# Optimization experiments

Measured on AMD Instinct MI355X. Metric: run time of the kernel, lower is better.

Reference implementation:

```python
import jax, jax.numpy as jnp
import numpy as np

BT = 64  # chunk size (BLOCK_SIZE_C)
EPS = 1e-06


def setup_inputs() -> dict:
    key = jax.random.key(0)
    k1, k2, k3, k4 = jax.random.split(key, 4)
    B, H, S, D = 4, 8, 4096, 128
    q = jax.random.normal(k1, (B, H, S, D), dtype=jnp.float32)
    k = jax.random.normal(k2, (B, H, S, D), dtype=jnp.float32)
    v = jax.random.normal(k3, (B, H, S, D), dtype=jnp.float32)
    beta = jax.random.uniform(k4, (B, H, S), dtype=jnp.float32)
    return {"q": q, "k": k, "v": v, "beta": beta}


def _chunk_gated_delta_fwd(q, k, v, beta):
    # Recurrence: S_t = beta_t * S_{t-1} + k_t (x) v_t ;  o_t = q_t @ S_t
    B, H, S, D = q.shape
    NC = S // BT
    f32 = jnp.float32
    qf = q.astype(f32).reshape(B, H, NC, BT, D)
    kf = k.astype(f32).reshape(B, H, NC, BT, D)
    vf = v.astype(f32).reshape(B, H, NC, BT, D)
    log_beta = jnp.log(beta.astype(f32).reshape(B, H, NC, BT) + EPS)
    cum = jnp.cumsum(log_beta, axis=-1)                     # [B,H,NC,BT]
    tot = cum[..., -1]                                      # [B,H,NC]
    decay_from_start = jnp.exp(cum)                         # [B,H,NC,BT]
    decay_to_end = jnp.exp(tot[..., None] - cum)            # [B,H,NC,BT]
    causal = jnp.tril(jnp.ones((BT, BT), dtype=bool))
    decay_matrix = jnp.exp(cum[..., :, None] - cum[..., None, :])  # [B,H,NC,BT,BT]
    decay_masked = jnp.where(causal, decay_matrix, 0.0)
    # intra-chunk contribution (fully parallel across chunks)
    qk = jnp.einsum('bhcid,bhcjd->bhcij', qf, kf)
    out_intra = jnp.einsum('bhcij,bhcjd->bhcid', qk * decay_masked, vf)
    # per-chunk state-update term: (k * decay_to_end)^T @ v
    upd = jnp.einsum('bhcid,bhcie->bhcde', kf * decay_to_end[..., None], vf)
    # sequential inter-chunk recurrence over chunks
    def step(state, xs):
        qc, dfs_c, tot_c, upd_c = xs
        out_inter = jnp.einsum('bhid,bhde->bhie', qc * dfs_c[..., None], state)
        new_state = state * jnp.exp(tot_c)[..., None, None] + upd_c
        return new_state, out_inter
    xs = (jnp.moveaxis(qf, 2, 0), jnp.moveaxis(decay_from_start, 2, 0),
          jnp.moveaxis(tot, 2, 0), jnp.moveaxis(upd, 2, 0))
    state0 = jnp.zeros((B, H, D, D), dtype=f32)
    _, out_inter = jax.lax.scan(step, state0, xs)           # [NC,B,H,BT,D]
    out = out_intra + jnp.moveaxis(out_inter, 0, 2)
    return out.reshape(B, H, S, D).astype(q.dtype)


def reference(q, k, v, beta):
    return _chunk_gated_delta_fwd(q, k, v, beta)
```

## Files before the change

kernel.cpp:

```cpp
#include <hip/hip_runtime.h>
#include <hip/hip_bf16.h>
#include <math.h>

#define Gp  32
#define Sp  4096
#define Dp  128
#define BTp 64
#define NCp 64

typedef __attribute__((ext_vector_type(8))) short bf16x8;
typedef __attribute__((ext_vector_type(4))) float f32x4;

#define MFMA(a,b,c) __builtin_amdgcn_mfma_f32_16x16x32_bf16((a),(b),(c),0,0,0)

#define TSWZ(d, slot) ((((slot) ^ (((d) & 15) >> 1)) << 3))

__device__ inline unsigned pack2(float lo, float hi) {
    __hip_bfloat162 h = __float22bfloat162_rn(make_float2(lo, hi));
    union { __hip_bfloat162 v; unsigned u; } t; t.v = h; return t.u;
}
__device__ inline float bflo(unsigned u) { union { unsigned u; float f; } t; t.u = u << 16; return t.f; }
__device__ inline float bfhi(unsigned u) { union { unsigned u; float f; } t; t.u = u & 0xffff0000u; return t.f; }

__global__ __launch_bounds__(256, 3) void gdn_intra(
    const float* __restrict__ q, const float* __restrict__ k,
    const float* __restrict__ v, const float* __restrict__ beta,
    float* __restrict__ out, unsigned short* __restrict__ upd,
    float* __restrict__ tot_buf, float* __restrict__ dfs_buf)
{
    __shared__ unsigned short s_k [64 * 128];
    __shared__ unsigned short s_vt[128 * 64];
    __shared__ unsigned short s_kt[128 * 64];

    const int blk = blockIdx.x, g = blk >> 6, c = blk & 63;
    const int tid = threadIdx.x, lane = tid & 63, w = tid >> 6;
    const int m16 = lane & 15, quad = lane >> 4;
    const size_t base  = ((size_t)g * Sp + (size_t)c * BTp) * Dp;
    const size_t bbase = (size_t)g * Sp + (size_t)c * BTp;

    float x = logf(beta[bbase + lane] + 1e-6f);
    #pragma unroll
    for (int off = 1; off < 64; off <<= 1) {
        float n = __shfl_up(x, off, 64);
        if (lane >= off) x += n;
    }
    const float tot = __shfl(x, 63, 64);
    const float dte_own = expf(tot - x);
    if (tid < 64) dfs_buf[bbase + lane] = expf(x);
    if (tid == 63) tot_buf[g * NCp + c] = tot;

    bf16x8 qf[4];
    {
        const float* qrow = q + base + (size_t)(16 * w + m16) * Dp + quad * 8;
        #pragma unroll
        for (int ks = 0; ks < 4; ++ks) {
            const float4 a = *(const float4*)(qrow + ks * 32);
            const float4 b = *(const float4*)(qrow + ks * 32 + 4);
            union { bf16x8 v; unsigned ui[4]; } t;
            t.ui[0] = pack2(a.x, a.y); t.ui[1] = pack2(a.z, a.w);
            t.ui[2] = pack2(b.x, b.y); t.ui[3] = pack2(b.z, b.w);
            qf[ks] = t.v;
        }
    }

    #pragma unroll
    for (int it = 0; it < 8; ++it) {
        const int idx = (it * 256 + tid) * 4;
        const int i = idx >> 7, d = idx & 127;
        const float4 kv = *(const float4*)(k + base + (size_t)i * Dp + d);
        const int ad = i * 128 + (((d >> 3) ^ (i & 15)) << 3) + (d & 7);
        uint2 pw; pw.x = pack2(kv.x, kv.y); pw.y = pack2(kv.z, kv.w);
        *(uint2*)&s_k[ad] = pw;
    }

    #pragma unroll
    for (int it = 0; it < 2; ++it) {
        const int dd = 2 * (tid & 63);
        const int i  = 32 * it + 8 * w;
        float2 lv[8], lk[8];
        #pragma unroll
        for (int r = 0; r < 8; ++r) {
            lv[r] = *(const float2*)(v + base + (size_t)(i + r) * Dp + dd);
            lk[r] = *(const float2*)(k + base + (size_t)(i + r) * Dp + dd);
        }
        float dt[8];
        #pragma unroll
        for (int r = 0; r < 8; ++r) dt[r] = __shfl(dte_own, i + r, 64);
        const int sl = TSWZ(dd, i >> 3);
        uint4 t0, t1;
        t0.x = pack2(lv[0].x, lv[1].x); t0.y = pack2(lv[2].x, lv[3].x);
        t0.z = pack2(lv[4].x, lv[5].x); t0.w = pack2(lv[6].x, lv[7].x);
        t1.x = pack2(lv[0].y, lv[1].y); t1.y = pack2(lv[2].y, lv[3].y);
        t1.z = pack2(lv[4].y, lv[5].y); t1.w = pack2(lv[6].y, lv[7].y);
        *(uint4*)&s_vt[dd * 64 + sl]       = t0;
        *(uint4*)&s_vt[(dd + 1) * 64 + sl] = t1;
        t0.x = pack2(lk[0].x * dt[0], lk[1].x * dt[1]); t0.y = pack2(lk[2].x * dt[2], lk[3].x * dt[3]);
        t0.z = pack2(lk[4].x * dt[4], lk[5].x * dt[5]); t0.w = pack2(lk[6].x * dt[6], lk[7].x * dt[7]);
        t1.x = pack2(lk[0].y * dt[0], lk[1].y * dt[1]); t1.y = pack2(lk[2].y * dt[2], lk[3].y * dt[3]);
        t1.z = pack2(lk[4].y * dt[4], lk[5].y * dt[5]); t1.w = pack2(lk[6].y * dt[6], lk[7].y * dt[7]);
        *(uint4*)&s_kt[dd * 64 + sl]       = t0;
        *(uint4*)&s_kt[(dd + 1) * 64 + sl] = t1;
    }

    __syncthreads();

    f32x4 accP[4] = {};
    #pragma unroll
    for (int nt = 0; nt < 4; ++nt) {
        if (nt <= w) {
            #pragma unroll
            for (int ks = 0; ks < 4; ++ks) {
                const bf16x8 kf = *(const bf16x8*)&s_k[(16 * nt + m16) * 128 + (((quad + 4 * ks) ^ m16) << 3)];
                accP[nt] = MFMA(kf, qf[ks], accP[nt]);
            }
        }
    }

    const float ci = __shfl(x, 16 * w + m16, 64);
    unsigned p_pk[4][2];
    #pragma unroll
    for (int nt = 0; nt < 4; ++nt) { p_pk[nt][0] = 0u; p_pk[nt][1] = 0u; }
    #pragma unroll
    for (int nt = 0; nt < 4; ++nt) {
        if (nt <= w) {
            float pm[4];
            #pragma unroll
            for (int r = 0; r < 4; ++r) {
                const int j = 16 * nt + 4 * quad + r;
                const float cj = __shfl(x, j, 64);
                float val = accP[nt][r] * expf(ci - cj);
                if (nt == w) val = (16 * w + m16 >= j) ? val : 0.f;
                pm[r] = val;
            }
            p_pk[nt][0] = pack2(pm[0], pm[1]);
            p_pk[nt][1] = pack2(pm[2], pm[3]);
        }
    }

    bf16x8 af[2];
    #pragma unroll
    for (int ks = 0; ks < 2; ++ks) {
        if (ks <= (w >> 1)) {
            union { bf16x8 v; unsigned ui[4]; } t;
            #pragma unroll
            for (int m = 0; m < 4; ++m) {
                const int src = m16 + 16 * (2 * (quad & 1) + (m >> 1));
                const unsigned aA = (unsigned)__shfl((int)p_pk[2 * ks][m & 1], src, 64);
                const unsigned aB = (unsigned)__shfl((int)p_pk[2 * ks + 1][m & 1], src, 64);
                t.ui[m] = (quad >> 1) ? aB : aA;
            }
            af[ks] = t.v;
        }
    }

    {
        f32x4 accU[2][8] = {};
        #pragma unroll
        for (int ks = 0; ks < 2; ++ks) {
            const int sw = TSWZ(m16, quad + 4 * ks);
            const bf16x8 b0 = *(const bf16x8*)&s_vt[(16 * (2 * w)     + m16) * 64 + sw];
            const bf16x8 b1 = *(const bf16x8*)&s_vt[(16 * (2 * w + 1) + m16) * 64 + sw];
            #pragma unroll
            for (int nt = 0; nt < 8; ++nt) {
                const bf16x8 a = *(const bf16x8*)&s_kt[(16 * nt + m16) * 64 + sw];
                accU[0][nt] = MFMA(a, b0, accU[0][nt]);
                accU[1][nt] = MFMA(a, b1, accU[1][nt]);
            }
        }
        unsigned short* ub = upd + (size_t)blk * Dp * Dp;
        #pragma unroll
        for (int mt = 0; mt < 2; ++mt) {
            const int e = 16 * (2 * w + mt) + m16;
            #pragma unroll
            for (int nt = 0; nt < 8; ++nt) {
                uint2 pw;
                pw.x = pack2(accU[mt][nt][0], accU[mt][nt][1]);
                pw.y = pack2(accU[mt][nt][2], accU[mt][nt][3]);
                *(uint2*)&ub[(size_t)e * Dp + 16 * nt + 4 * quad] = pw;
            }
        }
    }

    {
        f32x4 accO[8] = {};
        #pragma unroll
        for (int ks = 0; ks < 2; ++ks) {
            if (ks <= (w >> 1)) {
                const int sw = TSWZ(m16, quad + 4 * ks);
                #pragma unroll
                for (int nt = 0; nt < 8; ++nt) {
                    const bf16x8 a = *(const bf16x8*)&s_vt[(16 * nt + m16) * 64 + sw];
                    accO[nt] = MFMA(a, af[ks], accO[nt]);
                }
            }
        }
        const int i = 16 * w + m16;
        #pragma unroll
        for (int nt = 0; nt < 8; ++nt) {
            float4 st;
            st.x = accO[nt][0]; st.y = accO[nt][1];
            st.z = accO[nt][2]; st.w = accO[nt][3];
            *(float4*)&out[base + (size_t)i * Dp + 16 * nt + 4 * quad] = st;
        }
    }
}

__global__ __launch_bounds__(128) void gdn_scan(
    unsigned short* __restrict__ upd, const float* __restrict__ tot_buf)
{
    const int g = blockIdx.x >> 4, slab = blockIdx.x & 15, tid = threadIdx.x;
    __shared__ float s_e[NCp];
    if (tid < NCp) s_e[tid] = expf(tot_buf[g * NCp + tid]);
    __syncthreads();
    uint4* b = (uint4*)(upd + (size_t)g * NCp * Dp * Dp) + slab * 128 + tid;
    float s0 = 0.f, s1 = 0.f, s2 = 0.f, s3 = 0.f;
    float s4 = 0.f, s5 = 0.f, s6 = 0.f, s7 = 0.f;
    uint4 pf[4];
    #pragma unroll
    for (int j = 0; j < 4; ++j) pf[j] = b[(size_t)j * 2048];
    #pragma unroll
    for (int cc = 0; cc < NCp; ++cc) {
        const uint4 cur = pf[cc & 3];
        if (cc + 4 < NCp) pf[cc & 3] = b[(size_t)(cc + 4) * 2048];
        const float e = s_e[cc];
        uint4 stq;
        stq.x = pack2(s0, s1); stq.y = pack2(s2, s3);
        stq.z = pack2(s4, s5); stq.w = pack2(s6, s7);
        b[(size_t)cc * 2048] = stq;
        s0 = s0 * e + bflo(cur.x); s1 = s1 * e + bfhi(cur.x);
        s2 = s2 * e + bflo(cur.y); s3 = s3 * e + bfhi(cur.y);
        s4 = s4 * e + bflo(cur.z); s5 = s5 * e + bfhi(cur.z);
        s6 = s6 * e + bflo(cur.w); s7 = s7 * e + bfhi(cur.w);
    }
}

__global__ __launch_bounds__(256) void gdn_inter(
    const float* __restrict__ q, const unsigned short* __restrict__ state,
    const float* __restrict__ dfs_buf, float* __restrict__ out)
{
    const int blk = blockIdx.x, g = blk >> 6, c = blk & 63;
    const int tid = threadIdx.x, lane = tid & 63, w = tid >> 6;
    const int m16 = lane & 15, quad = lane >> 4;
    const size_t base  = ((size_t)g * Sp + (size_t)c * BTp) * Dp;
    const size_t bbase = (size_t)g * Sp + (size_t)c * BTp;
    const unsigned short* sb = state + (size_t)blk * Dp * Dp;
    const int i = 16 * w + m16;

    const float scale = dfs_buf[bbase + i];
    bf16x8 qf[4];
    const float* qrow = q + base + (size_t)i * Dp + quad * 8;
    #pragma unroll
    for (int ks = 0; ks < 4; ++ks) {
        const float4 a = *(const float4*)(qrow + ks * 32);
        const float4 b = *(const float4*)(qrow + ks * 32 + 4);
        union { bf16x8 v; unsigned ui[4]; } t;
        t.ui[0] = pack2(a.x * scale, a.y * scale);
        t.ui[1] = pack2(a.z * scale, a.w * scale);
        t.ui[2] = pack2(b.x * scale, b.y * scale);
        t.ui[3] = pack2(b.z * scale, b.w * scale);
        qf[ks] = t.v;
    }

    float4 ov[8];
    #pragma unroll
    for (int nt = 0; nt < 8; ++nt)
        ov[nt] = *(const float4*)&out[base + (size_t)i * Dp + 16 * nt + 4 * quad];

    f32x4 acc[8] = {};
    #pragma unroll
    for (int ks = 0; ks < 4; ++ks) {
        bf16x8 afr[8];
        #pragma unroll
        for (int nt = 0; nt < 8; ++nt)
            afr[nt] = *(const bf16x8*)(sb + (16 * nt + m16) * Dp + quad * 8 + ks * 32);
        #pragma unroll
        for (int nt = 0; nt < 8; ++nt)
            acc[nt] = MFMA(afr[nt], qf[ks], acc[nt]);
    }
    #pragma unroll
    for (int nt = 0; nt < 8; ++nt) {
        float4 st;
        st.x = ov[nt].x + acc[nt][0]; st.y = ov[nt].y + acc[nt][1];
        st.z = ov[nt].z + acc[nt][2]; st.w = ov[nt].w + acc[nt][3];
        *(float4*)&out[base + (size_t)i * Dp + 16 * nt + 4 * quad] = st;
    }
}

extern "C" void kernel_launch(void* const* d_in, const int* in_sizes, int n_in,
                              void* d_out, int out_size, void* d_ws, size_t ws_size,
                              hipStream_t stream) {
    const float* q    = (const float*)d_in[0];
    const float* k    = (const float*)d_in[1];
    const float* v    = (const float*)d_in[2];
    const float* beta = (const float*)d_in[3];
    float* out = (float*)d_out;

    unsigned short* upd = (unsigned short*)d_ws;
    float* tot_buf = (float*)(upd + (size_t)Gp * NCp * Dp * Dp);
    float* dfs_buf = tot_buf + Gp * NCp;

    gdn_intra<<<Gp * NCp, 256, 0, stream>>>(q, k, v, beta, out, upd, tot_buf, dfs_buf);
    gdn_scan <<<Gp * 16, 128, 0, stream>>>(upd, tot_buf);
    gdn_inter<<<Gp * NCp, 256, 0, stream>>>(q, upd, dfs_buf, out);
}
```

Before: 315.6 us.

## Split beta prefix-scan into own kernel, batch loads, store intra output as bf16

Moves the log-beta cumulative scan and decay computation into a separate small kernel that writes cum, dfs and dte buffers. The intra kernel can then issue all k/v/q loads up front without waiting on the scan, and it reads k only once instead of twice. When the workspace is large enough, the intra-chunk output is written as a bf16 scratch buffer and read back by the inter kernel, which roughly halves that round-trip traffic. The costs are an extra kernel launch, more registers held in flight, and lower precision in the intra output.

```diff
diff --git a/kernel.cpp b/kernel.cpp
--- a/kernel.cpp
+++ b/kernel.cpp
@@ -22,11 +22,34 @@
 __device__ inline float bflo(unsigned u) { union { unsigned u; float f; } t; t.u = u << 16; return t.f; }
 __device__ inline float bfhi(unsigned u) { union { unsigned u; float f; } t; t.u = u & 0xffff0000u; return t.f; }
 
+__global__ __launch_bounds__(256) void gdn_beta(
+    const float* __restrict__ beta, float* __restrict__ cum_buf,
+    float* __restrict__ dte_buf, float* __restrict__ dfs_buf,
+    float* __restrict__ tot_buf)
+{
+    const int tid = threadIdx.x, lane = tid & 63, w = tid >> 6;
+    const int cc = blockIdx.x * 4 + w;
+    const int g = cc >> 6, c = cc & 63;
+    const size_t bbase = (size_t)g * Sp + (size_t)c * BTp;
+    float x = logf(beta[bbase + lane] + 1e-6f);
+    #pragma unroll
+    for (int off = 1; off < 64; off <<= 1) {
+        float n = __shfl_up(x, off, 64);
+        if (lane >= off) x += n;
+    }
+    const float tot = __shfl(x, 63, 64);
+    cum_buf[bbase + lane] = x;
+    dfs_buf[bbase + lane] = expf(x);
+    dte_buf[bbase + lane] = expf(tot - x);
+    if (lane == 63) tot_buf[g * NCp + c] = tot;
+}
+
 __global__ __launch_bounds__(256, 3) void gdn_intra(
     const float* __restrict__ q, const float* __restrict__ k,
-    const float* __restrict__ v, const float* __restrict__ beta,
-    float* __restrict__ out, unsigned short* __restrict__ upd,
-    float* __restrict__ tot_buf, float* __restrict__ dfs_buf)
+    const float* __restrict__ v, const float* __restrict__ cum_buf,
+    const float* __restrict__ dte_buf,
+    float* __restrict__ out, unsigned short* __restrict__ outi,
+    unsigned short* __restrict__ upd)
 {
     __shared__ unsigned short s_k [64 * 128];
     __shared__ unsigned short s_vt[128 * 64];
@@ -38,68 +61,78 @@
     const size_t base  = ((size_t)g * Sp + (size_t)c * BTp) * Dp;
     const size_t bbase = (size_t)g * Sp + (size_t)c * BTp;
 
-    float x = logf(beta[bbase + lane] + 1e-6f);
-    #pragma unroll
-    for (int off = 1; off < 64; off <<= 1) {
-        float n = __shfl_up(x, off, 64);
-        if (lane >= off) x += n;
-    }
-    const float tot = __shfl(x, 63, 64);
-    const float dte_own = expf(tot - x);
-    if (tid < 64) dfs_buf[bbase + lane] = expf(x);
-    if (tid == 63) tot_buf[g * NCp + c] = tot;
+    const float x = cum_buf[bbase + lane];
+
+    const int dd = 4 * (tid & 31);
+    const int rg = tid >> 5;
+    const int i0 = 8 * rg;
+    const float* kp = k + base + (size_t)i0 * Dp + dd;
+    const float* vp = v + base + (size_t)i0 * Dp + dd;
+    float4 kx[8], vx[8];
+    #pragma unroll
+    for (int r = 0; r < 8; ++r) kx[r] = *(const float4*)(kp + (size_t)r * Dp);
+    #pragma unroll
+    for (int r = 0; r < 8; ++r) vx[r] = *(const float4*)(vp + (size_t)r * Dp);
+    const float4 dt0 = *(const float4*)(dte_buf + bbase + i0);
+    const float4 dt1 = *(const float4*)(dte_buf + bbase + i0 + 4);
+
+    const float* qrow = q + base + (size_t)(16 * w + m16) * Dp + quad * 8;
+    float4 qa[4], qb[4];
+    #pragma unroll
+    for (int ks = 0; ks < 4; ++ks) {
+        qa[ks] = *(const float4*)(qrow + ks * 32);
+        qb[ks] = *(const float4*)(qrow + ks * 32 + 4);
+    }
+
+    #pragma unroll
+    for (int r = 0; r < 8; ++r) {
+        const int i = i0 + r;
+        const int ad = i * 128 + (((dd >> 3) ^ (i & 15)) << 3) + (dd & 7);
+        uint2 pw; pw.x = pack2(kx[r].x, kx[r].y); pw.y = pack2(kx[r].z, kx[r].w);
+        *(uint2*)&s_k[ad] = pw;
+    }
+
+    {
+        uint4 t;
+        t.x = pack2(vx[0].x, vx[1].x); t.y = pack2(vx[2].x, vx[3].x);
+        t.z = pack2(vx[4].x, vx[5].x); t.w = pack2(vx[6].x, vx[7].x);
+        *(uint4*)&s_vt[(dd + 0) * 64 + TSWZ(dd + 0, rg)] = t;
+        t.x = pack2(vx[0].y, vx[1].y); t.y = pack2(vx[2].y, vx[3].y);
+        t.z = pack2(vx[4].y, vx[5].y); t.w = pack2(vx[6].y, vx[7].y);
+        *(uint4*)&s_vt[(dd + 1) * 64 + TSWZ(dd + 1, rg)] = t;
+        t.x = pack2(vx[0].z, vx[1].z); t.y = pack2(vx[2].z, vx[3].z);
+        t.z = pack2(vx[4].z, vx[5].z); t.w = pack2(vx[6].z, vx[7].z);
+        *(uint4*)&s_vt[(dd + 2) * 64 + TSWZ(dd + 2, rg)] = t;
+        t.x = pack2(vx[0].w, vx[1].w); t.y = pack2(vx[2].w, vx[3].w);
+        t.z = pack2(vx[4].w, vx[5].w); t.w = pack2(vx[6].w, vx[7].w);
+        *(uint4*)&s_vt[(dd + 3) * 64 + TSWZ(dd + 3, rg)] = t;
+    }
+
+    {
+        const float d0 = dt0.x, d1 = dt0.y, d2 = dt0.z, d3 = dt0.w;
+        const float d4 = dt1.x, d5 = dt1.y, d6 = dt1.z, d7 = dt1.w;
+        uint4 t;
+        t.x = pack2(kx[0].x * d0, kx[1].x * d1); t.y = pack2(kx[2].x * d2, kx[3].x * d3);
+        t.z = pack2(kx[4].x * d4, kx[5].x * d5); t.w = pack2(kx[6].x * d6, kx[7].x * d7);
+        *(uint4*)&s_kt[(dd + 0) * 64 + TSWZ(dd + 0, rg)] = t;
+        t.x = pack2(kx[0].y * d0, kx[1].y * d1); t.y = pack2(kx[2].y * d2, kx[3].y * d3);
+        t.z = pack2(kx[4].y * d4, kx[5].y * d5); t.w = pack2(kx[6].y * d6, kx[7].y * d7);
+        *(uint4*)&s_kt[(dd + 1) * 64 + TSWZ(dd + 1, rg)] = t;
+        t.x = pack2(kx[0].z * d0, kx[1].z * d1); t.y = pack2(kx[2].z * d2, kx[3].z * d3);
+        t.z = pack2(kx[4].z * d4, kx[5].z * d5); t.w = pack2(kx[6].z * d6, kx[7].z * d7);
+        *(uint4*)&s_kt[(dd + 2) * 64 + TSWZ(dd + 2, rg)] = t;
+        t.x = pack2(kx[0].w * d0, kx[1].w * d1); t.y = pack2(kx[2].w * d2, kx[3].w * d3);
+        t.z = pack2(kx[4].w * d4, kx[5].w * d5); t.w = pack2(kx[6].w * d6, kx[7].w * d7);
+        *(uint4*)&s_kt[(dd + 3) * 64 + TSWZ(dd + 3, rg)] = t;
+    }
 
     bf16x8 qf[4];
-    {
-        const float* qrow = q + base + (size_t)(16 * w + m16) * Dp + quad * 8;
-        #pragma unroll
-        for (int ks = 0; ks < 4; ++ks) {
-            const float4 a = *(const float4*)(qrow + ks * 32);
-            const float4 b = *(const float4*)(qrow + ks * 32 + 4);
-            union { bf16x8 v; unsigned ui[4]; } t;
-            t.ui[0] = pack2(a.x, a.y); t.ui[1] = pack2(a.z, a.w);
-            t.ui[2] = pack2(b.x, b.y); t.ui[3] = pack2(b.z, b.w);
-            qf[ks] = t.v;
-        }
-    }
-
-    #pragma unroll
-    for (int it = 0; it < 8; ++it) {
-        const int idx = (it * 256 + tid) * 4;
-        const int i = idx >> 7, d = idx & 127;
-        const float4 kv = *(const float4*)(k + base + (size_t)i * Dp + d);
-        const int ad = i * 128 + (((d >> 3) ^ (i & 15)) << 3) + (d & 7);
-        uint2 pw; pw.x = pack2(kv.x, kv.y); pw.y = pack2(kv.z, kv.w);
-        *(uint2*)&s_k[ad] = pw;
-    }
-
-    #pragma unroll
-    for (int it = 0; it < 2; ++it) {
-        const int dd = 2 * (tid & 63);
-        const int i  = 32 * it + 8 * w;
-        float2 lv[8], lk[8];
-        #pragma unroll
-        for (int r = 0; r < 8; ++r) {
-            lv[r] = *(const float2*)(v + base + (size_t)(i + r) * Dp + dd);
-            lk[r] = *(const float2*)(k + base + (size_t)(i + r) * Dp + dd);
-        }
-        float dt[8];
-        #pragma unroll
-        for (int r = 0; r < 8; ++r) dt[r] = __shfl(dte_own, i + r, 64);
-        const int sl = TSWZ(dd, i >> 3);
-        uint4 t0, t1;
-        t0.x = pack2(lv[0].x, lv[1].x); t0.y = pack2(lv[2].x, lv[3].x);
-        t0.z = pack2(lv[4].x, lv[5].x); t0.w = pack2(lv[6].x, lv[7].x);
-        t1.x = pack2(lv[0].y, lv[1].y); t1.y = pack2(lv[2].y, lv[3].y);
-        t1.z = pack2(lv[4].y, lv[5].y); t1.w = pack2(lv[6].y, lv[7].y);
-        *(uint4*)&s_vt[dd * 64 + sl]       = t0;
-        *(uint4*)&s_vt[(dd + 1) * 64 + sl] = t1;
-        t0.x = pack2(lk[0].x * dt[0], lk[1].x * dt[1]); t0.y = pack2(lk[2].x * dt[2], lk[3].x * dt[3]);
-        t0.z = pack2(lk[4].x * dt[4], lk[5].x * dt[5]); t0.w = pack2(lk[6].x * dt[6], lk[7].x * dt[7]);
-        t1.x = pack2(lk[0].y * dt[0], lk[1].y * dt[1]); t1.y = pack2(lk[2].y * dt[2], lk[3].y * dt[3]);
-        t1.z = pack2(lk[4].y * dt[4], lk[5].y * dt[5]); t1.w = pack2(lk[6].y * dt[6], lk[7].y * dt[7]);
-        *(uint4*)&s_kt[dd * 64 + sl]       = t0;
-        *(uint4*)&s_kt[(dd + 1) * 64 + sl] = t1;
+    #pragma unroll
+    for (int ks = 0; ks < 4; ++ks) {
+        union { bf16x8 v; unsigned ui[4]; } t;
+        t.ui[0] = pack2(qa[ks].x, qa[ks].y); t.ui[1] = pack2(qa[ks].z, qa[ks].w);
+        t.ui[2] = pack2(qb[ks].x, qb[ks].y); t.ui[3] = pack2(qb[ks].z, qb[ks].w);
+        qf[ks] = t.v;
     }
 
     __syncthreads();
@@ -195,12 +228,22 @@
             }
         }
         const int i = 16 * w + m16;
-        #pragma unroll
-        for (int nt = 0; nt < 8; ++nt) {
-            float4 st;
-            st.x = accO[nt][0]; st.y = accO[nt][1];
-            st.z = accO[nt][2]; st.w = accO[nt][3];
-            *(float4*)&out[base + (size_t)i * Dp + 16 * nt + 4 * quad] = st;
+        if (outi) {
+            #pragma unroll
+            for (int nt = 0; nt < 8; ++nt) {
+                uint2 pw;
+                pw.x = pack2(accO[nt][0], accO[nt][1]);
+                pw.y = pack2(accO[nt][2], accO[nt][3]);
+                *(uint2*)&outi[base + (size_t)i * Dp + 16 * nt + 4 * quad] = pw;
+            }
+        } else {
+            #pragma unroll
+            for (int nt = 0; nt < 8; ++nt) {
+                float4 st;
+                st.x = accO[nt][0]; st.y = accO[nt][1];
+                st.z = accO[nt][2]; st.w = accO[nt][3];
+                *(float4*)&out[base + (size_t)i * Dp + 16 * nt + 4 * quad] = st;
+            }
         }
     }
 }
@@ -236,7 +279,8 @@
 
 __global__ __launch_bounds__(256) void gdn_inter(
     const float* __restrict__ q, const unsigned short* __restrict__ state,
-    const float* __restrict__ dfs_buf, float* __restrict__ out)
+    const float* __restrict__ dfs_buf, const unsigned short* __restrict__ outi,
+    float* __restrict__ out)
 {
     const int blk = blockIdx.x, g = blk >> 6, c = blk & 63;
     const int tid = threadIdx.x, lane = tid & 63, w = tid >> 6;
@@ -261,10 +305,21 @@
         qf[ks] = t.v;
     }
 
-    float4 ov[8];
-    #pragma unroll
-    for (int nt = 0; nt < 8; ++nt)
-        ov[nt] = *(const float4*)&out[base + (size_t)i * Dp + 16 * nt + 4 * quad];
+    float ovf[8][4];
+    if (outi) {
+        #pragma unroll
+        for (int nt = 0; nt < 8; ++nt) {
+            const uint2 pw = *(const uint2*)&outi[base + (size_t)i * Dp + 16 * nt + 4 * quad];
+            ovf[nt][0] = bflo(pw.x); ovf[nt][1] = bfhi(pw.x);
+            ovf[nt][2] = bflo(pw.y); ovf[nt][3] = bfhi(pw.y);
+        }
+    } else {
+        #pragma unroll
+        for (int nt = 0; nt < 8; ++nt) {
+            const float4 o = *(const float4*)&out[base + (size_t)i * Dp + 16 * nt + 4 * quad];
+            ovf[nt][0] = o.x; ovf[nt][1] = o.y; ovf[nt][2] = o.z; ovf[nt][3] = o.w;
+        }
+    }
 
     f32x4 acc[8] = {};
     #pragma unroll
@@ -280,8 +335,8 @@
     #pragma unroll
     for (int nt = 0; nt < 8; ++nt) {
         float4 st;
-        st.x = ov[nt].x + acc[nt][0]; st.y = ov[nt].y + acc[nt][1];
-        st.z = ov[nt].z + acc[nt][2]; st.w = ov[nt].w + acc[nt][3];
+        st.x = ovf[nt][0] + acc[nt][0]; st.y = ovf[nt][1] + acc[nt][1];
+        st.z = ovf[nt][2] + acc[nt][2]; st.w = ovf[nt][3] + acc[nt][3];
         *(float4*)&out[base + (size_t)i * Dp + 16 * nt + 4 * quad] = st;
     }
 }
@@ -298,8 +353,14 @@
     unsigned short* upd = (unsigned short*)d_ws;
     float* tot_buf = (float*)(upd + (size_t)Gp * NCp * Dp * Dp);
     float* dfs_buf = tot_buf + Gp * NCp;
-
-    gdn_intra<<<Gp * NCp, 256, 0, stream>>>(q, k, v, beta, out, upd, tot_buf, dfs_buf);
+    float* cum_buf = dfs_buf + (size_t)Gp * Sp;
+    float* dte_buf = cum_buf + (size_t)Gp * Sp;
+    unsigned short* outi = (unsigned short*)(dte_buf + (size_t)Gp * Sp);
+    const size_t need = (size_t)((char*)(outi + (size_t)Gp * Sp * Dp) - (char*)d_ws);
+    if (ws_size < need) outi = nullptr;
+
+    gdn_beta <<<Gp * NCp / 4, 256, 0, stream>>>(beta, cum_buf, dte_buf, dfs_buf, tot_buf);
+    gdn_intra<<<Gp * NCp, 256, 0, stream>>>(q, k, v, cum_buf, dte_buf, out, outi, upd);
     gdn_scan <<<Gp * 16, 128, 0, stream>>>(upd, tot_buf);
-    gdn_inter<<<Gp * NCp, 256, 0, stream>>>(q, upd, dfs_buf, out);
-}
+    gdn_inter<<<Gp * NCp, 256, 0, stream>>>(q, upd, dfs_buf, outi, out);
+}
```

New measurement: 302.1 us. 1.04x faster.
